# Optimization experiments

Measured on AMD Instinct MI355X. Metric: run time of the kernel, lower is better.

Reference implementation:

```python
import jax, jax.numpy as jnp
import numpy as np

B, R, IMG_DIM, TAG_DIM = 256, 36, 2048, 768
BOX_LEN = 15
POS_EMBED = 200
POS_SIZE = 16 * 16 + 1  # 257
EMBED_SIZE = 1024
EPS_NORM = 1e-8
EPS_ATTN = 1e-6


def setup_inputs() -> dict:
    key = jax.random.key(0)
    ks = jax.random.split(key, 8)
    images = jax.random.normal(ks[0], (B, R, IMG_DIM), dtype=jnp.float32)
    images_tag = jax.random.normal(ks[1], (B, R, TAG_DIM), dtype=jnp.float32)
    # boxes: first 15 entries are integer position indices, last 15 are weights
    box_idx = jax.random.randint(ks[2], (B, R, BOX_LEN), 0, POS_SIZE).astype(jnp.float32)
    box_w = jax.random.uniform(ks[3], (B, R, BOX_LEN), dtype=jnp.float32)
    boxes = jnp.concatenate([box_idx, box_w], axis=-1)  # [B,R,30]
    # parameters (xavier-uniform-like for linears, normal for embedding)
    pos_emb = jax.random.normal(ks[4], (POS_SIZE, POS_EMBED), dtype=jnp.float32)
    fan = (IMG_DIM + TAG_DIM) + POS_EMBED
    r1 = np.sqrt(6.0) / np.sqrt(fan)
    attn_W = jax.random.uniform(ks[5], (POS_EMBED, IMG_DIM + TAG_DIM), dtype=jnp.float32, minval=-r1, maxval=r1)
    fc_in = IMG_DIM + POS_EMBED + TAG_DIM
    r2 = np.sqrt(6.0) / np.sqrt(fc_in + EMBED_SIZE)
    fc_W = jax.random.uniform(ks[6], (EMBED_SIZE, fc_in), dtype=jnp.float32, minval=-r2, maxval=r2)
    fc_b = jnp.zeros((EMBED_SIZE,), dtype=jnp.float32)
    return {"images": images, "images_tag": images_tag, "boxes": boxes,
            "pos_emb": pos_emb, "attn_W": attn_W, "fc_W": fc_W, "fc_b": fc_b}


def reference(images, images_tag, boxes, pos_emb, attn_W, fc_W, fc_b):
    half = boxes.shape[2] // 2  # 15
    idx = boxes[..., :half].astype(jnp.int32)        # [B,R,15] position indices
    box_w = boxes[..., half:]                        # [B,R,15] weights
    img_tag = jnp.concatenate([images, images_tag], axis=-1)  # [B,R,2816]
    box_emb = pos_emb[idx]                           # [B,R,15,200]
    # posi_attn (vectorized over batch instead of python loop)
    region = jnp.einsum('brd,ed->bre', img_tag, attn_W)        # [B,R,200]
    scores = jnp.einsum('bre,brke->brk', region, box_emb)      # [B,R,15]
    attn = jax.nn.softmax(jnp.tanh(scores), axis=-1)
    attn = attn * box_w
    attn = attn / (jnp.sum(attn, axis=-1, keepdims=True) + EPS_ATTN)
    box_feat = jnp.einsum('brk,brke->bre', attn, box_emb)      # [B,R,200]
    # original uses .data -> detached attention output
    box_feat = jax.lax.stop_gradient(box_feat)
    image_position = jnp.concatenate([images, box_feat, images_tag], axis=-1)  # [B,R,3016]
    features = jnp.einsum('brd,ed->bre', image_position, fc_W) + fc_b
    norm = jnp.sqrt(jnp.sum(features ** 2, axis=-1, keepdims=True)) + EPS_NORM
    return features / norm
```

## Files before the change

kernel.cpp:

```cpp
#include <hip/hip_runtime.h>


#define M_TOT 9216
#define K1    2816
#define K2    3072
#define ES    1024
#define REGN  (9216L * 208)

typedef __attribute__((ext_vector_type(8))) short bf16x8;
typedef __attribute__((ext_vector_type(4))) float floatx4;

static __device__ __forceinline__ unsigned short f2bf(float f) {
    unsigned int u = __float_as_uint(f);
    u += 0x7fffu + ((u >> 16) & 1u);
    return (unsigned short)(u >> 16);
}

static __device__ __forceinline__ uint4 pack8(const float4 f0, const float4 f1) {
    uint4 pk;
    pk.x = (unsigned)f2bf(f0.x) | ((unsigned)f2bf(f0.y) << 16);
    pk.y = (unsigned)f2bf(f0.z) | ((unsigned)f2bf(f0.w) << 16);
    pk.z = (unsigned)f2bf(f1.x) | ((unsigned)f2bf(f1.y) << 16);
    pk.w = (unsigned)f2bf(f1.z) | ((unsigned)f2bf(f1.w) << 16);
    return pk;
}

static __device__ __forceinline__ void cvt8(const float* __restrict__ g,
                                            unsigned short* __restrict__ d) {
    *(uint4*)d = pack8(*(const float4*)g, *(const float4*)(g + 4));
}

static __device__ __forceinline__ void gl16(const void* g, const void* l) {
    __builtin_amdgcn_global_load_lds(
        (const __attribute__((address_space(1))) unsigned int*)g,
        (__attribute__((address_space(3))) unsigned int*)(unsigned int)(unsigned long long)l,
        16, 0, 0);
}

#define NC_WF  (1024 * 384)
#define NC_WA  ( 208 * 352)
__global__ __launch_bounds__(256) void k_prep_w(
    const float* __restrict__ attn_W,
    const float* __restrict__ fc_W,
    unsigned short* __restrict__ Wa,
    unsigned short* __restrict__ Wf)
{
    const int u = blockIdx.x * 256 + threadIdx.x;
    uint4 z; z.x = z.y = z.z = z.w = 0u;
    if (u < NC_WF) {
        const int r = u / 384;
        const int dc = (u - r * 384) * 8;
        unsigned short* d = Wf + (long)r * K2 + dc;
        if (dc < 2248)      cvt8(fc_W + (long)r * 3016 + dc, d);
        else if (dc < 2304) *(uint4*)d = z;
        else                cvt8(fc_W + (long)r * 3016 + (dc - 56), d);
    } else if (u < NC_WF + NC_WA) {
        const int v = u - NC_WF;
        const int r = v / 352;
        const int c = (v - r * 352) * 8;
        if (r < 200) cvt8(attn_W + (long)r * K1 + c, Wa + (long)r * K1 + c);
        else         *(uint4*)(Wa + (long)r * K1 + c) = z;
    }
}

__global__ __launch_bounds__(256, 5) void k_gemm1(
    const float* __restrict__ images,
    const float* __restrict__ tag,
    const unsigned short* __restrict__ Wa,
    unsigned short* __restrict__ Abf,
    float* __restrict__ regP)
{
    __shared__ __align__(16) unsigned short lds[14336];
    unsigned short* ldsA = lds;
    unsigned short* ldsB = lds + 1024;

    const int t = threadIdx.x;
    const int lane = t & 63;
    const int w = t >> 6;
    const int quad = lane >> 4;
    const int ln15 = lane & 15;
    const int x7 = ln15 & 7;
    const int bid = blockIdx.x;
    const int m0 = (bid >> 1) * 16;
    const int kh = bid & 1;
    const int kbase = kh * 1408;
    const int lrow = lane >> 3;
    const int schunk = (lane & 7) ^ lrow;
    const int nj = (w == 0) ? 4 : 3;

    const bool stA = (t < 128);
    const int sr = t >> 3;
    const int sgl = t & 7;
    const int aslot = sr * 64 + ((sgl ^ (sr & 7)) << 3);

    floatx4 acc[4] = {};
    float4 v0, v1;

    if (stA) {
        const float* src = (kbase < 2048)
            ? images + (long)(m0 + sr) * 2048 + kbase + sgl * 8
            : tag + (long)(m0 + sr) * 768 + (kbase - 2048) + sgl * 8;
        v0 = *(const float4*)src;
        v1 = *(const float4*)(src + 4);
    }

    for (int kt = 0; kt < 22; ++kt) {
        const int kb = kbase + kt * 64;
        if (stA) {
            const uint4 pk = pack8(v0, v1);
            *(uint4*)&ldsA[aslot] = pk;
            const int acol = kb + ((kb >= 2048) ? 256 : 0);
            *(uint4*)(Abf + (long)(m0 + sr) * K2 + acol + sgl * 8) = pk;
            if (kt < 21) {
                const int kn = kb + 64;
                const float* src = (kn < 2048)
                    ? images + (long)(m0 + sr) * 2048 + kn + sgl * 8
                    : tag + (long)(m0 + sr) * 768 + (kn - 2048) + sgl * 8;
                v0 = *(const float4*)src;
                v1 = *(const float4*)(src + 4);
            }
        }
#pragma unroll
        for (int i = 0; i < 7; ++i) {
            const int u = w + i * 4;
            if (u < 26)
                gl16(Wa + (long)(u * 8 + lrow) * K1 + kb + schunk * 8, ldsB + u * 512);
        }
        __syncthreads();
#pragma unroll
        for (int s = 0; s < 2; ++s) {
            const int g = s * 4 + quad;
            const int co = (g ^ x7) << 3;
            const bf16x8 a = *(const bf16x8*)&ldsA[ln15 * 64 + co];
#pragma unroll
            for (int jj = 0; jj < 4; ++jj) {
                if (jj < nj) {
                    const int j = w + jj * 4;
                    const bf16x8 b = *(const bf16x8*)&ldsB[(j * 16 + ln15) * 64 + co];
                    acc[jj] = __builtin_amdgcn_mfma_f32_16x16x32_bf16(a, b, acc[jj], 0, 0, 0);
                }
            }
        }
        __syncthreads();
    }

    float* rp = regP + (long)kh * REGN;
#pragma unroll
    for (int jj = 0; jj < 4; ++jj) {
        if (jj < nj) {
            const int j = w + jj * 4;
#pragma unroll
            for (int r = 0; r < 4; ++r)
                rp[(long)(m0 + quad * 4 + r) * 208 + j * 16 + ln15] = acc[jj][r];
        }
    }
}

__global__ __launch_bounds__(256, 4) void k_attn(
    const float* __restrict__ regP,
    const float* __restrict__ boxes,
    const float* __restrict__ pos_emb,
    unsigned short* __restrict__ Abf)
{
    const int t = threadIdx.x;
    const int lane = t & 63;
    const int w = t >> 6;
    const int m = blockIdx.x * 4 + w;

    const float* r0 = regP + (long)m * 208;
    const float* r1 = r0 + REGN;
    float rv[4];
#pragma unroll
    for (int c = 0; c < 4; ++c) {
        const int e = lane + c * 64;
        rv[c] = (e < 200) ? (r0[e] + r1[e]) : 0.0f;
    }
    const float* bx = boxes + (long)m * 30;
    int idx[15]; float bw[15], sc_[15];
#pragma unroll
    for (int k = 0; k < 15; ++k) {
        int ii = (int)bx[k];
        idx[k] = (ii < 0) ? 0 : (ii > 256 ? 256 : ii);
        bw[k] = bx[15 + k];
    }
#pragma unroll
    for (int k = 0; k < 15; ++k) {
        const float* em = pos_emb + (long)idx[k] * 200;
        float p = 0.0f;
#pragma unroll
        for (int c = 0; c < 4; ++c) {
            const int e = lane + c * 64;
            if (e < 200) p += rv[c] * em[e];
        }
        for (int off = 32; off; off >>= 1) p += __shfl_xor(p, off, 64);
        sc_[k] = p;
    }
    float mx = -1e30f;
#pragma unroll
    for (int k = 0; k < 15; ++k) { sc_[k] = tanhf(sc_[k]); mx = fmaxf(mx, sc_[k]); }
    float Z = 0.0f, den = 0.0f, pk[15];
#pragma unroll
    for (int k = 0; k < 15; ++k) { pk[k] = __expf(sc_[k] - mx); Z += pk[k]; }
#pragma unroll
    for (int k = 0; k < 15; ++k) { pk[k] *= bw[k]; den += pk[k]; }
    den += 1e-6f * Z;
    const float inv = 1.0f / den;
    unsigned short* bo = Abf + (long)m * K2 + 2048;
#pragma unroll
    for (int c = 0; c < 4; ++c) {
        const int e = lane + c * 64;
        float o = 0.0f;
        if (e < 200) {
#pragma unroll
            for (int k = 0; k < 15; ++k) o += pk[k] * pos_emb[(long)idx[k] * 200 + e];
            o *= inv;
        }
        bo[e] = f2bf(o);
    }
}

__global__ __launch_bounds__(256, 4) void k_gemm2(
    const unsigned short* __restrict__ Abf,
    const unsigned short* __restrict__ Wf,
    float* __restrict__ dout)
{
    __shared__ __align__(16) unsigned short ldsA[128 * 64];
    __shared__ __align__(16) unsigned short ldsB[128 * 64];
    const int t = threadIdx.x;
    const int lane = t & 63;
    const int w = t >> 6;
    const int quad = lane >> 4;
    const int ln15 = lane & 15;
    const int x7 = ln15 & 7;
    const int n0 = blockIdx.x * 128;
    const int m0 = blockIdx.y * 128;
    const int lrow = lane >> 3;
    const int schunk = (lane & 7) ^ lrow;
    const int wm = (w & 1) * 64;
    const int wn = (w >> 1) * 64;

    floatx4 acc[4][4] = {};

    for (int kt = 0; kt < 48; ++kt) {
        const int kb = kt * 64;
#pragma unroll
        for (int i = 0; i < 4; ++i) {
            const int u = w * 4 + i;
            const int r = u * 8 + lrow;
            gl16(Abf + (long)(m0 + r) * K2 + kb + schunk * 8, ldsA + u * 512);
            gl16(Wf  + (long)(n0 + r) * K2 + kb + schunk * 8, ldsB + u * 512);
        }
        __syncthreads();
#pragma unroll
        for (int s = 0; s < 2; ++s) {
            const int g = s * 4 + quad;
            const int co = (g ^ x7) << 3;
            bf16x8 a[4], b[4];
#pragma unroll
            for (int i = 0; i < 4; ++i)
                a[i] = *(const bf16x8*)&ldsA[(wm + i * 16 + ln15) * 64 + co];
#pragma unroll
            for (int j = 0; j < 4; ++j)
                b[j] = *(const bf16x8*)&ldsB[(wn + j * 16 + ln15) * 64 + co];
#pragma unroll
            for (int i = 0; i < 4; ++i)
#pragma unroll
                for (int j = 0; j < 4; ++j)
                    acc[i][j] = __builtin_amdgcn_mfma_f32_16x16x32_bf16(a[i], b[j], acc[i][j], 0, 0, 0);
        }
        __syncthreads();
    }
#pragma unroll
    for (int i = 0; i < 4; ++i)
#pragma unroll
        for (int j = 0; j < 4; ++j) {
            const int row = m0 + wm + i * 16 + quad * 4;
            const int col = n0 + wn + j * 16 + ln15;
#pragma unroll
            for (int r = 0; r < 4; ++r)
                dout[(long)(row + r) * ES + col] = acc[i][j][r];
        }
}

__global__ __launch_bounds__(256) void k_norm(
    float* __restrict__ dout,
    const float* __restrict__ bias)
{
    __shared__ float red[4];
    const int m = blockIdx.x;
    const int t = threadIdx.x;
    float* f = dout + (long)m * ES + t * 4;
    float4 v = *(const float4*)f;
    const float4 bs = *(const float4*)(bias + t * 4);
    v.x += bs.x; v.y += bs.y; v.z += bs.z; v.w += bs.w;
    float ss = v.x * v.x + v.y * v.y + v.z * v.z + v.w * v.w;
    for (int off = 32; off; off >>= 1) ss += __shfl_xor(ss, off, 64);
    if ((t & 63) == 0) red[t >> 6] = ss;
    __syncthreads();
    const float total = red[0] + red[1] + red[2] + red[3];
    const float inv = 1.0f / (sqrtf(total) + 1e-8f);
    float4 o;
    o.x = v.x * inv; o.y = v.y * inv; o.z = v.z * inv; o.w = v.w * inv;
    *(float4*)f = o;
}

extern "C" void kernel_launch(void* const* d_in, const int* in_sizes, int n_in,
                              void* d_out, int out_size, void* d_ws, size_t ws_size,
                              hipStream_t stream) {
    const float* images  = (const float*)d_in[0];
    const float* tag     = (const float*)d_in[1];
    const float* boxes   = (const float*)d_in[2];
    const float* pos_emb = (const float*)d_in[3];
    const float* attn_W  = (const float*)d_in[4];
    const float* fc_W    = (const float*)d_in[5];
    const float* fc_b    = (const float*)d_in[6];
    float* out = (float*)d_out;

    unsigned short* Abf = (unsigned short*)d_ws;
    unsigned short* Wf  = Abf + (size_t)M_TOT * K2;
    unsigned short* Wa  = Wf  + (size_t)ES * K2;
    float* regP = (float*)(Wa + (size_t)208 * K1);

    k_prep_w<<<1822, 256, 0, stream>>>(attn_W, fc_W, Wa, Wf);
    k_gemm1 <<<1152, 256, 0, stream>>>(images, tag, Wa, Abf, regP);
    k_attn  <<<2304, 256, 0, stream>>>(regP, boxes, pos_emb, Abf);
    k_gemm2 <<<dim3(8, 72), 256, 0, stream>>>(Abf, Wf, out);
    k_norm  <<<M_TOT, 256, 0, stream>>>(out, fc_b);
}
```

Before: 328.0 us.

## Retile both GEMMs: 64-row split-K4 gemm1 with atomics, 144x128 gemm2 tiles

gemm1 now uses 64-row M tiles and a 4-way K split, so each block reuses the attention-weight tile across 4 waves. Partial sums are combined with atomicAdd into a zeroed regP buffer instead of two separate partial buffers, and k_attn is simplified to read one buffer. gemm2 moves to 144x128 tiles with 6 waves (384 threads), giving 512 blocks, which fits the 256-CU device better than the old 576. The costs are atomic contention, an extra memset, nondeterministic float summation order and higher register use in both kernels.

```diff
diff --git a/kernel.cpp b/kernel.cpp
--- a/kernel.cpp
+++ b/kernel.cpp
@@ -5,7 +5,6 @@
 #define K1    2816
 #define K2    3072
 #define ES    1024
-#define REGN  (9216L * 208)
 
 typedef __attribute__((ext_vector_type(8))) short bf16x8;
 typedef __attribute__((ext_vector_type(4))) float floatx4;
@@ -63,16 +62,15 @@
     }
 }
 
-__global__ __launch_bounds__(256, 5) void k_gemm1(
+__global__ __launch_bounds__(256, 4) void k_gemm1(
     const float* __restrict__ images,
     const float* __restrict__ tag,
     const unsigned short* __restrict__ Wa,
     unsigned short* __restrict__ Abf,
     float* __restrict__ regP)
 {
-    __shared__ __align__(16) unsigned short lds[14336];
-    unsigned short* ldsA = lds;
-    unsigned short* ldsB = lds + 1024;
+    __shared__ __align__(16) unsigned short ldsA[64 * 64];
+    __shared__ __align__(16) unsigned short ldsB[208 * 64];
 
     const int t = threadIdx.x;
     const int lane = t & 63;
@@ -81,44 +79,41 @@
     const int ln15 = lane & 15;
     const int x7 = ln15 & 7;
     const int bid = blockIdx.x;
-    const int m0 = (bid >> 1) * 16;
-    const int kh = bid & 1;
-    const int kbase = kh * 1408;
+    const int m0 = (bid >> 2) * 64;
+    const int kh = bid & 3;
+    const int kbase = kh * 704;
     const int lrow = lane >> 3;
     const int schunk = (lane & 7) ^ lrow;
-    const int nj = (w == 0) ? 4 : 3;
-
-    const bool stA = (t < 128);
-    const int sr = t >> 3;
-    const int sgl = t & 7;
-    const int aslot = sr * 64 + ((sgl ^ (sr & 7)) << 3);
-
-    floatx4 acc[4] = {};
-    float4 v0, v1;
-
-    if (stA) {
-        const float* src = (kbase < 2048)
-            ? images + (long)(m0 + sr) * 2048 + kbase + sgl * 8
-            : tag + (long)(m0 + sr) * 768 + (kbase - 2048) + sgl * 8;
-        v0 = *(const float4*)src;
-        v1 = *(const float4*)(src + 4);
-    }
-
-    for (int kt = 0; kt < 22; ++kt) {
+
+    const int rA = t >> 3;
+    const int gA = t & 7;
+    const int aslot0 = rA * 64 + ((gA ^ (rA & 7)) << 3);
+    const int aslot1 = (rA + 32) * 64 + ((gA ^ (rA & 7)) << 3);
+
+    floatx4 acc[13] = {};
+    float4 p0a, p0b, p1a, p1b;
+
+    {
+        const float* s0 = (kbase < 2048)
+            ? images + (long)(m0 + rA) * 2048 + kbase + gA * 8
+            : tag + (long)(m0 + rA) * 768 + (kbase - 2048) + gA * 8;
+        const float* s1 = (kbase < 2048)
+            ? images + (long)(m0 + rA + 32) * 2048 + kbase + gA * 8
+            : tag + (long)(m0 + rA + 32) * 768 + (kbase - 2048) + gA * 8;
+        p0a = *(const float4*)s0; p0b = *(const float4*)(s0 + 4);
+        p1a = *(const float4*)s1; p1b = *(const float4*)(s1 + 4);
+    }
+
+    for (int kt = 0; kt < 11; ++kt) {
         const int kb = kbase + kt * 64;
-        if (stA) {
-            const uint4 pk = pack8(v0, v1);
-            *(uint4*)&ldsA[aslot] = pk;
+        {
+            const uint4 k0 = pack8(p0a, p0b);
+            const uint4 k1 = pack8(p1a, p1b);
+            *(uint4*)&ldsA[aslot0] = k0;
+            *(uint4*)&ldsA[aslot1] = k1;
             const int acol = kb + ((kb >= 2048) ? 256 : 0);
-            *(uint4*)(Abf + (long)(m0 + sr) * K2 + acol + sgl * 8) = pk;
-            if (kt < 21) {
-                const int kn = kb + 64;
-                const float* src = (kn < 2048)
-                    ? images + (long)(m0 + sr) * 2048 + kn + sgl * 8
-                    : tag + (long)(m0 + sr) * 768 + (kn - 2048) + sgl * 8;
-                v0 = *(const float4*)src;
-                v1 = *(const float4*)(src + 4);
-            }
+            *(uint4*)(Abf + (long)(m0 + rA) * K2 + acol + gA * 8) = k0;
+            *(uint4*)(Abf + (long)(m0 + rA + 32) * K2 + acol + gA * 8) = k1;
         }
 #pragma unroll
         for (int i = 0; i < 7; ++i) {
@@ -126,34 +121,38 @@
             if (u < 26)
                 gl16(Wa + (long)(u * 8 + lrow) * K1 + kb + schunk * 8, ldsB + u * 512);
         }
+        if (kt < 10) {
+            const int kn = kb + 64;
+            const float* s0 = (kn < 2048)
+                ? images + (long)(m0 + rA) * 2048 + kn + gA * 8
+                : tag + (long)(m0 + rA) * 768 + (kn - 2048) + gA * 8;
+            const float* s1 = (kn < 2048)
+                ? images + (long)(m0 + rA + 32) * 2048 + kn + gA * 8
+                : tag + (long)(m0 + rA + 32) * 768 + (kn - 2048) + gA * 8;
+            p0a = *(const float4*)s0; p0b = *(const float4*)(s0 + 4);
+            p1a = *(const float4*)s1; p1b = *(const float4*)(s1 + 4);
+        }
         __syncthreads();
 #pragma unroll
         for (int s = 0; s < 2; ++s) {
             const int g = s * 4 + quad;
             const int co = (g ^ x7) << 3;
-            const bf16x8 a = *(const bf16x8*)&ldsA[ln15 * 64 + co];
-#pragma unroll
-            for (int jj = 0; jj < 4; ++jj) {
-                if (jj < nj) {
-                    const int j = w + jj * 4;
-                    const bf16x8 b = *(const bf16x8*)&ldsB[(j * 16 + ln15) * 64 + co];
-                    acc[jj] = __builtin_amdgcn_mfma_f32_16x16x32_bf16(a, b, acc[jj], 0, 0, 0);
-                }
+            const bf16x8 a = *(const bf16x8*)&ldsA[(w * 16 + ln15) * 64 + co];
+#pragma unroll
+            for (int j = 0; j < 13; ++j) {
+                const bf16x8 b = *(const bf16x8*)&ldsB[(j * 16 + ln15) * 64 + co];
+                acc[j] = __builtin_amdgcn_mfma_f32_16x16x32_bf16(a, b, acc[j], 0, 0, 0);
             }
         }
         __syncthreads();
     }
 
-    float* rp = regP + (long)kh * REGN;
-#pragma unroll
-    for (int jj = 0; jj < 4; ++jj) {
-        if (jj < nj) {
-            const int j = w + jj * 4;
-#pragma unroll
-            for (int r = 0; r < 4; ++r)
-                rp[(long)(m0 + quad * 4 + r) * 208 + j * 16 + ln15] = acc[jj][r];
-        }
-    }
+#pragma unroll
+    for (int j = 0; j < 13; ++j)
+#pragma unroll
+        for (int r = 0; r < 4; ++r)
+            atomicAdd(&regP[(long)(m0 + w * 16 + quad * 4 + r) * 208 + j * 16 + ln15],
+                      acc[j][r]);
 }
 
 __global__ __launch_bounds__(256, 4) void k_attn(
@@ -168,12 +167,11 @@
     const int m = blockIdx.x * 4 + w;
 
     const float* r0 = regP + (long)m * 208;
-    const float* r1 = r0 + REGN;
     float rv[4];
 #pragma unroll
     for (int c = 0; c < 4; ++c) {
         const int e = lane + c * 64;
-        rv[c] = (e < 200) ? (r0[e] + r1[e]) : 0.0f;
+        rv[c] = (e < 200) ? r0[e] : 0.0f;
     }
     const float* bx = boxes + (long)m * 30;
     int idx[15]; float bw[15], sc_[15];
@@ -219,12 +217,12 @@
     }
 }
 
-__global__ __launch_bounds__(256, 4) void k_gemm2(
+__global__ __launch_bounds__(384, 3) void k_gemm2(
     const unsigned short* __restrict__ Abf,
     const unsigned short* __restrict__ Wf,
     float* __restrict__ dout)
 {
-    __shared__ __align__(16) unsigned short ldsA[128 * 64];
+    __shared__ __align__(16) unsigned short ldsA[144 * 64];
     __shared__ __align__(16) unsigned short ldsB[128 * 64];
     const int t = threadIdx.x;
     const int lane = t & 63;
@@ -232,38 +230,42 @@
     const int quad = lane >> 4;
     const int ln15 = lane & 15;
     const int x7 = ln15 & 7;
-    const int n0 = blockIdx.x * 128;
-    const int m0 = blockIdx.y * 128;
+    const int nx = blockIdx.x & 7;
+    const int mx = blockIdx.x >> 3;
+    const int m0 = mx * 144;
+    const int n0 = nx * 128;
     const int lrow = lane >> 3;
     const int schunk = (lane & 7) ^ lrow;
-    const int wm = (w & 1) * 64;
-    const int wn = (w >> 1) * 64;
-
-    floatx4 acc[4][4] = {};
+    const int wm = (w % 3) * 48;
+    const int wn = (w / 3) * 64;
+
+    floatx4 acc[3][4] = {};
 
     for (int kt = 0; kt < 48; ++kt) {
         const int kb = kt * 64;
 #pragma unroll
-        for (int i = 0; i < 4; ++i) {
-            const int u = w * 4 + i;
-            const int r = u * 8 + lrow;
-            gl16(Abf + (long)(m0 + r) * K2 + kb + schunk * 8, ldsA + u * 512);
-            gl16(Wf  + (long)(n0 + r) * K2 + kb + schunk * 8, ldsB + u * 512);
+        for (int i = 0; i < 6; ++i) {
+            const int u = w + i * 6;
+            if (u < 18)
+                gl16(Abf + (long)(m0 + u * 8 + lrow) * K2 + kb + schunk * 8, ldsA + u * 512);
+            else if (u < 34)
+                gl16(Wf + (long)(n0 + (u - 18) * 8 + lrow) * K2 + kb + schunk * 8,
+                     ldsB + (u - 18) * 512);
         }
         __syncthreads();
 #pragma unroll
         for (int s = 0; s < 2; ++s) {
             const int g = s * 4 + quad;
             const int co = (g ^ x7) << 3;
-            bf16x8 a[4], b[4];
-#pragma unroll
-            for (int i = 0; i < 4; ++i)
+            bf16x8 a[3], b[4];
+#pragma unroll
+            for (int i = 0; i < 3; ++i)
                 a[i] = *(const bf16x8*)&ldsA[(wm + i * 16 + ln15) * 64 + co];
 #pragma unroll
             for (int j = 0; j < 4; ++j)
                 b[j] = *(const bf16x8*)&ldsB[(wn + j * 16 + ln15) * 64 + co];
 #pragma unroll
-            for (int i = 0; i < 4; ++i)
+            for (int i = 0; i < 3; ++i)
 #pragma unroll
                 for (int j = 0; j < 4; ++j)
                     acc[i][j] = __builtin_amdgcn_mfma_f32_16x16x32_bf16(a[i], b[j], acc[i][j], 0, 0, 0);
@@ -271,7 +273,7 @@
         __syncthreads();
     }
 #pragma unroll
-    for (int i = 0; i < 4; ++i)
+    for (int i = 0; i < 3; ++i)
 #pragma unroll
         for (int j = 0; j < 4; ++j) {
             const int row = m0 + wm + i * 16 + quad * 4;
@@ -322,8 +324,9 @@
     float* regP = (float*)(Wa + (size_t)208 * K1);
 
     k_prep_w<<<1822, 256, 0, stream>>>(attn_W, fc_W, Wa, Wf);
-    k_gemm1 <<<1152, 256, 0, stream>>>(images, tag, Wa, Abf, regP);
+    hipMemsetAsync(regP, 0, (size_t)M_TOT * 208 * sizeof(float), stream);
+    k_gemm1 <<<576, 256, 0, stream>>>(images, tag, Wa, Abf, regP);
     k_attn  <<<2304, 256, 0, stream>>>(regP, boxes, pos_emb, Abf);
-    k_gemm2 <<<dim3(8, 72), 256, 0, stream>>>(Abf, Wf, out);
+    k_gemm2 <<<512, 384, 0, stream>>>(Abf, Wf, out);
     k_norm  <<<M_TOT, 256, 0, stream>>>(out, fc_b);
 }
```

After: 307.5 us. 6.2% less time.
